# Performance work log

Hardware: AMD Instinct MI355X
Metric: run time of the kernel (lower is better)

The kernel has to match this reference:

```python
import jax, jax.numpy as jnp
import numpy as np

V = 30000   # vocab (from get_word_embedding default)
D = 640     # d_model
L = 6       # num_layers
H = 8       # num_heads
DH = D // H # head dim 80
FF = 4 * D  # ffn hidden 2560
BOS = 1
EOS = 2
LN_EPS = 1e-6


def _ln(x, s, b):
    m = x.mean(-1, keepdims=True)
    v = ((x - m) ** 2).mean(-1, keepdims=True)
    return (x - m) / jnp.sqrt(v + LN_EPS) * s + b


def _get_logits(tokens, seq_len, emb, Wq, bq, Wk, bk, Wv, bv, Wo, bo,
                ln1s, ln1b, W1, b1, W2, b2, ln2s, ln2b, lmW, lmb):
    # tokens: (B,S) int; seq_len: (B,) int
    B, S = tokens.shape
    h = emb[tokens]                                   # (B,S,D), no pos-enc / scaling in source
    look_ahead = jnp.triu(jnp.ones((S, S), jnp.float32), k=1)          # 1 = masked (TF-style)
    pad = (jnp.arange(S)[None, :] >= seq_len[:, None]).astype(jnp.float32)  # (B,S)
    mask = jnp.maximum(look_ahead[None, None, :, :], pad[:, None, None, :])  # (B,1,S,S)

    def layer(h, p):
        wq, bq_, wk, bk_, wv, bv_, wo, bo_, l1s, l1b, w1, b1_, w2, b2_, l2s, l2b = p
        q = (h @ wq + bq_).reshape(B, S, H, DH)
        k = (h @ wk + bk_).reshape(B, S, H, DH)
        v = (h @ wv + bv_).reshape(B, S, H, DH)
        scores = jnp.einsum('bqhd,bkhd->bhqk', q, k) / jnp.sqrt(jnp.float32(DH))
        scores = scores - mask * 1e9
        a = jax.nn.softmax(scores, axis=-1)
        o = jnp.einsum('bhqk,bkhd->bqhd', a, v).reshape(B, S, D) @ wo + bo_
        h = _ln(h + o, l1s, l1b)                      # post-LN residual
        f = jax.nn.relu(h @ w1 + b1_) @ w2 + b2_
        h = _ln(h + f, l2s, l2b)
        return h, None

    h, _ = jax.lax.scan(layer, h, (Wq, bq, Wk, bk, Wv, bv, Wo, bo,
                                   ln1s, ln1b, W1, b1, W2, b2, ln2s, ln2b))
    return h @ lmW + lmb                              # (B,S,V)


def setup_inputs() -> dict:
    key = jax.random.key(0)
    ks = jax.random.split(key, 12)
    std = 0.02

    def n(k, shape):
        return jax.random.normal(k, shape, jnp.float32) * std

    return {
        'initial_words': jax.random.randint(ks[0], (4, 8), 3, V, dtype=jnp.int32),
        'max_length': 32,
        'emb': n(ks[1], (V, D)),
        'Wq': n(ks[2], (L, D, D)), 'bq': jnp.zeros((L, D), jnp.float32),
        'Wk': n(ks[3], (L, D, D)), 'bk': jnp.zeros((L, D), jnp.float32),
        'Wv': n(ks[4], (L, D, D)), 'bv': jnp.zeros((L, D), jnp.float32),
        'Wo': n(ks[5], (L, D, D)), 'bo': jnp.zeros((L, D), jnp.float32),
        'ln1s': jnp.ones((L, D), jnp.float32), 'ln1b': jnp.zeros((L, D), jnp.float32),
        'W1': n(ks[6], (L, D, FF)), 'b1': jnp.zeros((L, FF), jnp.float32),
        'W2': n(ks[7], (L, FF, D)), 'b2': jnp.zeros((L, D), jnp.float32),
        'ln2s': jnp.ones((L, D), jnp.float32), 'ln2b': jnp.zeros((L, D), jnp.float32),
        'lmW': n(ks[8], (D, V)), 'lmb': jnp.zeros((V,), jnp.float32),
    }


def reference(initial_words, max_length, emb, Wq, bq, Wk, bk, Wv, bv, Wo, bo,
              ln1s, ln1b, W1, b1, W2, b2, ln2s, ln2b, lmW, lmb):
    B, init_len = initial_words.shape
    seq_len = jnp.full((B,), max_length, jnp.int32)
    S = max_length + 1  # BOS + max_length slots, as in the torch padding logic
    inp = (jnp.zeros((B, S), jnp.int32)
           .at[:, 0].set(BOS)
           .at[:, 1:1 + init_len].set(initial_words.astype(jnp.int32)))

    def cond(c):
        _inp, cl, tok = c
        return (cl + 1 <= max_length) & jnp.any(tok != EOS)

    def body(c):
        inp, cl, _tok = c
        logits = _get_logits(inp, seq_len, emb, Wq, bq, Wk, bk, Wv, bv, Wo, bo,
                             ln1s, ln1b, W1, b1, W2, b2, ln2s, ln2b, lmW, lmb)
        step_logits = jax.lax.dynamic_index_in_dim(logits, cl, axis=1, keepdims=False)
        tok = jnp.argmax(step_logits, axis=-1).astype(jnp.int32)
        inp = inp.at[:, cl + 1].set(tok)
        return (inp, cl + 1, tok)

    inp, _, _ = jax.lax.while_loop(
        cond, body,
        (inp, jnp.int32(init_len), jnp.full((B,), -100, jnp.int32)))
    return inp[:, 1:]
```

## Files before the change

### kernel.cpp

```cpp
#include <hip/hip_runtime.h>
#include <math.h>

#define B 4
#define SEQ 33
#define MAXLEN 32
#define D 640
#define NH 8
#define DH 80
#define NL 6
#define FF 2560
#define V 30000
#define INITLEN 8
#define NBLK 1024
#define NT 256
#define EOS_TOK 2
#define NPOS_P 9
#define NR_P 36
#define LM_NB 938

#define QKV_N 240
#define AW_B 240
#define AW_E 304
#define F1_B 304
#define F1_E 624
#define F2_B 624
#define F2_E 784

#define NFLAGS 1024
#define NSLOT 32
#define SLOT_U 16

#define VER(t,l) ((size_t)((t) * NL + (l)))

typedef float f4 __attribute__((ext_vector_type(4)));

struct Par {
  const int* iw;
  const float* emb;
  const float *Wq, *bq, *Wk, *bk, *Wv, *bv, *Wo, *bo;
  const float *ln1s, *ln1b, *W1, *b1, *W2, *b2, *ln2s, *ln2b, *lmW, *lmb;
  int* out;
};

__device__ __align__(256) float g_Kc[(size_t)NL * B * NH * SEQ * DH];
__device__ __align__(256) float g_Vc[(size_t)NL * B * NH * SEQ * DH];
__device__ __align__(256) float g_xv[(size_t)SEQ * NL * 2560];
__device__ __align__(256) float g_h1v[(size_t)SEQ * NL * 2560];
__device__ __align__(256) float g_qv[(size_t)SEQ * NL * 2560];
__device__ __align__(256) float g_opartv[(size_t)SEQ * NL * 20480];
__device__ __align__(256) float g_f1v[(size_t)SEQ * NL * 10240];
__device__ __align__(256) float g_f2v[(size_t)SEQ * NL * 5120];
__device__ __align__(256) float g_xlm[(size_t)SEQ * 2560];
__device__ __align__(256) int   g_tokv[SEQ * 64];
__device__ __align__(256) int   g_stopv[SEQ * 64];
__device__ float g_xp[NR_P * D];
__device__ float g_h1p[NR_P * D];
__device__ float g_qkvpP[(size_t)8 * 1920 * NR_P];
__device__ float g_qP[(size_t)NH * NR_P * DH];
__device__ float g_opartP[(size_t)NH * D * NR_P];
__device__ float g_f1pP[(size_t)8 * FF * NR_P];
__device__ float g_f2pP[(size_t)32 * D * NR_P];
__device__ unsigned long long g_keys[(size_t)NBLK * B];
__device__ int g_tokens[B * SEQ];
__device__ unsigned g_flags[(size_t)NFLAGS * NSLOT * SLOT_U];
__device__ unsigned g_arrive = 0;
__device__ unsigned g_gen = 0;

#define KCIDX(l,b,h,pos,j) (((((size_t)(l)*B+(b))*NH+(h))*SEQ+(pos))*DH+(j))

__device__ __forceinline__ float ldc(const float* p) {
  return __hip_atomic_load(p, __ATOMIC_RELAXED, __HIP_MEMORY_SCOPE_AGENT);
}
__device__ __forceinline__ void stc(float* p, float v) {
  __hip_atomic_store(p, v, __ATOMIC_RELAXED, __HIP_MEMORY_SCOPE_AGENT);
}
__device__ __forceinline__ int ldci(const int* p) {
  return __hip_atomic_load(p, __ATOMIC_RELAXED, __HIP_MEMORY_SCOPE_AGENT);
}
__device__ __forceinline__ void stci(int* p, int v) {
  __hip_atomic_store(p, v, __ATOMIC_RELAXED, __HIP_MEMORY_SCOPE_AGENT);
}
__device__ __forceinline__ void stcu64(unsigned long long* p, unsigned long long v) {
  __hip_atomic_store(p, v, __ATOMIC_RELAXED, __HIP_MEMORY_SCOPE_AGENT);
}
__device__ __forceinline__ void st4c(float* p, f4 v) {
  asm volatile("global_store_dwordx4 %0, %1, off sc1" :: "v"(p), "v"(v) : "memory");
}
__device__ __forceinline__ void ld4c_issue(f4& dst, const float* p) {
  asm volatile("global_load_dwordx4 %0, %1, off sc1" : "=v"(dst) : "v"(p) : "memory");
}
__device__ __forceinline__ void wait_vm() {
  asm volatile("s_waitcnt vmcnt(0)" ::: "memory");
  __builtin_amdgcn_sched_barrier(0);
}
__device__ __forceinline__ unsigned long long mk64(float lo, float hi) {
  return ((unsigned long long)__float_as_uint(hi) << 32) | (unsigned long long)__float_as_uint(lo);
}
__device__ __forceinline__ void keep(float x) { asm volatile("" :: "v"(x)); }

__device__ __forceinline__ void gsync_full() {
  __syncthreads();
  if (threadIdx.x == 0) {
    __threadfence();
    unsigned g = __hip_atomic_load(&g_gen, __ATOMIC_SEQ_CST, __HIP_MEMORY_SCOPE_AGENT);
    unsigned old = __hip_atomic_fetch_add(&g_arrive, 1u, __ATOMIC_SEQ_CST, __HIP_MEMORY_SCOPE_AGENT);
    if (old == NBLK - 1u) {
      __hip_atomic_store(&g_arrive, 0u, __ATOMIC_SEQ_CST, __HIP_MEMORY_SCOPE_AGENT);
      __hip_atomic_fetch_add(&g_gen, 1u, __ATOMIC_SEQ_CST, __HIP_MEMORY_SCOPE_AGENT);
    } else {
      while (__hip_atomic_load(&g_gen, __ATOMIC_RELAXED, __HIP_MEMORY_SCOPE_AGENT) == g)
        __builtin_amdgcn_s_sleep(2);
    }
    __threadfence();
  }
  __syncthreads();
}

__device__ __forceinline__ void stage_done(int idx) {
  asm volatile("s_waitcnt vmcnt(0)" ::: "memory");
  __syncthreads();
  if (threadIdx.x == 0) {
    __hip_atomic_fetch_add(
        &g_flags[((size_t)idx * NSLOT + (blockIdx.x & (NSLOT - 1))) * SLOT_U],
        1u, __ATOMIC_RELAXED, __HIP_MEMORY_SCOPE_AGENT);
  }
}

__device__ __forceinline__ void stage_wait(int idx, unsigned cnt) {
  if (threadIdx.x < 64) {
    const unsigned* base = &g_flags[(size_t)idx * NSLOT * SLOT_U];
    int spins = 0;
    for (;;) {
      unsigned v = 0u;
      if (threadIdx.x < NSLOT)
        v = __hip_atomic_load(base + (size_t)threadIdx.x * SLOT_U,
                              __ATOMIC_RELAXED, __HIP_MEMORY_SCOPE_AGENT);
      #pragma unroll
      for (int o = 16; o > 0; o >>= 1) v += __shfl_down(v, o, 64);
      v = __shfl(v, 0, 64);
      if (v >= cnt) break;
      if (spins < 16)       __builtin_amdgcn_s_sleep(1);
      else if (spins < 128) __builtin_amdgcn_s_sleep(8);
      else                  __builtin_amdgcn_s_sleep(32);
      ++spins;
    }
  }
  __syncthreads();
  asm volatile("" ::: "memory");
}

__device__ __forceinline__ float bred_sum(float v, float* s_red) {
  #pragma unroll
  for (int o = 32; o > 0; o >>= 1) v += __shfl_down(v, o, 64);
  __syncthreads();
  if ((threadIdx.x & 63) == 0) s_red[threadIdx.x >> 6] = v;
  __syncthreads();
  return s_red[0] + s_red[1] + s_red[2] + s_red[3];
}

__device__ void ln_inplace(float* row, const float* gam, const float* bet, float* s_red) {
  float ps = 0.f;
  for (int d = threadIdx.x; d < D; d += NT) ps += row[d];
  const float m = bred_sum(ps, s_red) * (1.0f / 640.0f);
  float pv = 0.f;
  for (int d = threadIdx.x; d < D; d += NT) { float t = row[d] - m; pv += t * t; }
  const float var = bred_sum(pv, s_red) * (1.0f / 640.0f);
  const float rstd = 1.0f / sqrtf(var + 1e-6f);
  for (int d = threadIdx.x; d < D; d += NT)
    row[d] = (row[d] - m) * rstd * gam[d] + bet[d];
  __syncthreads();
}

__device__ __forceinline__ void ln_wave(float* s_x, const float* gam, const float* bet) {
  const int tid = threadIdx.x, w = tid >> 6, lane = tid & 63;
  float ps = 0.f;
  for (int i = lane; i < D; i += 64) ps += s_x[w * 640 + i];
  #pragma unroll
  for (int o = 32; o > 0; o >>= 1) ps += __shfl_xor(ps, o, 64);
  const float mean = ps * (1.0f / 640.0f);
  float pv = 0.f;
  for (int i = lane; i < D; i += 64) { float d = s_x[w * 640 + i] - mean; pv += d * d; }
  #pragma unroll
  for (int o = 32; o > 0; o >>= 1) pv += __shfl_xor(pv, o, 64);
  const float rstd = 1.0f / sqrtf(pv * (1.0f / 640.0f) + 1e-6f);
  for (int i = lane; i < D; i += 64)
    s_x[w * 640 + i] = (s_x[w * 640 + i] - mean) * rstd * gam[i] + bet[i];
}

__device__ __forceinline__ void build_x2w(const Par& p, int t, int lsrc, float* s_x) {
  const int tid = threadIdx.x, w = tid >> 6, lane = tid & 63;
  const size_t ver = VER(t, lsrc);
  const float* h1 = g_h1v + ver * 2560 + w * 640;
  const float* fa = g_f2v + ver * 5120 + w * 640;
  const float* fb = g_f2v + ver * 5120 + 2560 + w * 640;
  const float* b2 = p.b2 + (size_t)lsrc * D;
  for (int c4 = lane; c4 < 160; c4 += 64) {
    f4 a = *(const f4*)&h1[c4 * 4];
    f4 b = *(const f4*)&fa[c4 * 4];
    f4 c = *(const f4*)&fb[c4 * 4];
    const float* bb = b2 + c4 * 4;
    f4 s = { a.x + b.x + c.x + bb[0], a.y + b.y + c.y + bb[1],
             a.z + b.z + c.z + bb[2], a.w + b.w + c.w + bb[3] };
    *(f4*)&s_x[w * 640 + c4 * 4] = s;
  }
  ln_wave(s_x, p.ln2s + (size_t)lsrc * D, p.ln2b + (size_t)lsrc * D);
}


__device__ void pf_QKV(const Par& p, int l) {
  const int tid = threadIdx.x;
  const int cg = (blockIdx.x & 7) * 30 + (blockIdx.x >> 3);
  const int m = cg / 80, colm0 = (cg % 80) * 8;
  const int ds = tid >> 3, c = tid & 7;
  const float* Wb = (m == 0 ? p.Wq : m == 1 ? p.Wk : p.Wv)
                    + (size_t)l * D * D + colm0 + c;
  float s = 0.f;
  #pragma unroll
  for (int j = 0; j < 20; ++j) s += Wb[(size_t)(ds + j * 32) * D];
  keep(s);
}

__device__ void pf_AW(const Par& p, int l) {
  const int idx = blockIdx.x - AW_B, h = idx >> 3, c = idx & 7, tid = threadIdx.x;
  if (tid < 240) {
    const int j = tid % 80, sub = tid / 80;
    const int col = c * 80 + j;
    const int d0 = sub * 27, d1 = (sub == 2) ? 80 : d0 + 27;
    const float* Wo = p.Wo + (size_t)l * D * D + col;
    float s = 0.f;
    for (int dd = d0; dd < d1; ++dd) s += Wo[(size_t)(h * 80 + dd) * D];
    keep(s);
  }
}

__device__ void pf_F1(const Par& p, int l) {
  const int tid = threadIdx.x;
  const int raw = blockIdx.x - F1_B;
  const int cg = (raw & 7) * 40 + (raw >> 3);
  const int col0 = cg * 8;
  const int ds = tid >> 3, c = tid & 7;
  const float* Wb = p.W1 + (size_t)l * D * FF + col0 + c;
  float s = 0.f;
  #pragma unroll
  for (int j = 0; j < 20; ++j) s += Wb[(size_t)(ds + j * 32) * FF];
  keep(s);
}

__device__ void pf_F2(const Par& p, int l) {
  const int idx = blockIdx.x - F2_B, tid = threadIdx.x;
  const int hf = idx / 80, craw = idx % 80;
  const int cg = (craw & 7) * 10 + (craw >> 3);
  const int col0 = cg * 8;
  const int ds = tid >> 3, c = tid & 7;
  const float* Wb = p.W2 + (size_t)l * FF * D + (size_t)hf * 1280 * D + col0 + c;
  float s = 0.f;
  #pragma unroll
  for (int kb = 0; kb < 40; ++kb) s += Wb[(size_t)(ds + kb * 32) * D];
  keep(s);
}

__device__ void pf_LM(const Par& p) {
  const int bid = blockIdx.x, tid = threadIdx.x;
  const int xcd = bid & 7, jj = bid >> 3;
  const int chunk = (xcd < 2 ? xcd * 118 : 236 + (xcd - 2) * 117) + jj;
  const int sg = tid >> 5, cj = tid & 31;
  const int col = chunk * 32 + cj;
  if (col < V) {
    const float* W = p.lmW + (size_t)sg * 80 * V + col;
    float s = 0.f;
    for (int kb = 0; kb < 80; ++kb) s += W[(size_t)kb * V];
    keep(s);
  }
}


__device__ void st_QKV(const Par& p, int l, int t, float* s_x, float* s_t, float* s_r) {
  const int tid = threadIdx.x;
  const int cg = (blockIdx.x & 7) * 30 + (blockIdx.x >> 3);
  const int m = cg / 80, colm0 = (cg % 80) * 8;
  const int w = tid >> 6, lane = tid & 63;
  if (l == 0) {
    const int tok = g_tokv[t * 64 + w];
    for (int c4 = lane; c4 < 160; c4 += 64)
      *(f4*)&s_x[w * 640 + c4 * 4] = *(const f4*)&p.emb[(size_t)tok * D + c4 * 4];
  } else {
    build_x2w(p, t, l - 1, s_x);
  }
  __syncthreads();
  if (cg == 0) {
    const size_t xo = VER(t, l) * 2560;
    for (int i = tid; i < 640; i += NT)
      st4c(&g_xv[xo + (size_t)i * 4], *(f4*)&s_x[i * 4]);
  }
  const int ds = tid >> 3, c = tid & 7;
  const float* Wb = (m == 0 ? p.Wq : m == 1 ? p.Wk : p.Wv)
                    + (size_t)l * D * D + colm0 + c;
  float a0 = 0, a1 = 0, a2 = 0, a3 = 0;
  {
    float wv[20];
    #pragma unroll
    for (int j = 0; j < 20; ++j) wv[j] = Wb[(size_t)(ds + j * 32) * D];
    #pragma unroll
    for (int j = 0; j < 20; ++j) {
      const int dd = ds + j * 32;
      a0 = fmaf(s_x[dd],        wv[j], a0);
      a1 = fmaf(s_x[640 + dd],  wv[j], a1);
      a2 = fmaf(s_x[1280 + dd], wv[j], a2);
      a3 = fmaf(s_x[1920 + dd], wv[j], a3);
    }
  }
  { f4 av = { a0, a1, a2, a3 }; *(f4*)&s_t[c * 132 + ds * 4] = av; }
  __syncthreads();
  if (tid < 32) {
    const int c2 = tid >> 2, b = tid & 3;
    float v = 0.f;
    #pragma unroll
    for (int d2 = 0; d2 < 32; ++d2) v += s_t[c2 * 132 + d2 * 4 + b];
    v += (m == 0 ? p.bq : m == 1 ? p.bk : p.bv)[(size_t)l * D + colm0 + c2];
    s_r[c2 * 4 + b] = v;
  }
  __syncthreads();
  if (m == 0) {
    if (tid < 8) {
      f4 v = { s_r[tid * 4], s_r[tid * 4 + 1], s_r[tid * 4 + 2], s_r[tid * 4 + 3] };
      st4c(&g_qv[VER(t, l) * 2560 + (size_t)(colm0 + tid) * 4], v);
    }
  } else {
    const int h = colm0 / 80, j0 = colm0 % 80;
    if (tid < 8) {
      const int b = tid >> 1, cq4 = (tid & 1) * 4;
      f4 v = { s_r[(cq4+0)*4+b], s_r[(cq4+1)*4+b], s_r[(cq4+2)*4+b], s_r[(cq4+3)*4+b] };
      float* cache = (m == 1) ? g_Kc : g_Vc;
      st4c(&cache[KCIDX(l, b, h, t, j0 + cq4)], v);
    }
  }
}

__device__ void st_AW(const Par& p, int l, int t,
                      float* s_q, float* s_sc, float* s_o, float* s_wo) {
  const int idx = blockIdx.x - AW_B, h = idx >> 3, c = idx & 7, tid = threadIdx.x;
  const size_t qo = VER(t, l) * 2560;
  if (tid < 80) {
    f4 q = *(const f4*)&g_qv[qo + (size_t)(h * 80 + tid) * 4];
    s_q[tid] = q.x; s_q[80 + tid] = q.y; s_q[160 + tid] = q.z; s_q[240 + tid] = q.w;
  }
  __syncthreads();
  const int nk = t + 1;
  for (int task = tid; task < 4 * nk; task += NT) {
    const int b = task / nk, kp = task % nk;
    const float* qq = s_q + b * 80;
    const f4* kk = (const f4*)&g_Kc[KCIDX(l, b, h, kp, 0)];
    float sd = 0.f;
    #pragma unroll
    for (int j4 = 0; j4 < 20; ++j4) {
      f4 k4 = kk[j4];
      sd += qq[j4*4+0]*k4.x + qq[j4*4+1]*k4.y + qq[j4*4+2]*k4.z + qq[j4*4+3]*k4.w;
    }
    s_sc[b * 33 + kp] = sd / 8.94427190999915878564f;
  }
  __syncthreads();
  if (tid < 4) {
    const int b = tid;
    float m = -1e30f;
    for (int k = 0; k < nk; ++k) m = fmaxf(m, s_sc[b * 33 + k]);
    float sum = 0.f;
    for (int k = 0; k < nk; ++k) { float e = expf(s_sc[b * 33 + k] - m); s_sc[b * 33 + k] = e; sum += e; }
    s_sc[132 + b] = 1.0f / sum;
  }
  __syncthreads();
  if (tid < 80) {
    const int b = tid / 20, j4 = tid % 20;
    f4 acc = { 0.f, 0.f, 0.f, 0.f };
    for (int kp = 0; kp < nk; ++kp) {
      f4 v = *(const f4*)&g_Vc[KCIDX(l, b, h, kp, j4 * 4)];
      const float wgt = s_sc[b * 33 + kp];
      acc.x += wgt * v.x; acc.y += wgt * v.y; acc.z += wgt * v.z; acc.w += wgt * v.w;
    }
    const float r = s_sc[132 + b];
    f4 o = { acc.x * r, acc.y * r, acc.z * r, acc.w * r };
    *(f4*)&s_o[b * 80 + j4 * 4] = o;
  }
  __syncthreads();
  if (tid < 240) {
    const int j = tid % 80, sub = tid / 80;
    const int col = c * 80 + j;
    const int d0 = sub * 27, d1 = (sub == 2) ? 80 : d0 + 27;
    const float* Wo = p.Wo + (size_t)l * D * D + col;
    float a0 = 0, a1 = 0, a2 = 0, a3 = 0;
    #pragma unroll 9
    for (int dd = d0; dd < d1; ++dd) {
      const float w = Wo[(size_t)(h * 80 + dd) * D];
      a0 += s_o[0*80+dd] * w; a1 += s_o[80+dd] * w;
      a2 += s_o[160+dd] * w; a3 += s_o[240+dd] * w;
    }
    float* tp = s_wo + (j * 3 + sub) * 4;
    tp[0] = a0; tp[1] = a1; tp[2] = a2; tp[3] = a3;
  }
  __syncthreads();
  if (tid < 80) {
    const int b = tid / 20, cq = tid % 20;
    f4 v;
    #pragma unroll
    for (int i = 0; i < 4; ++i) {
      const int j = cq * 4 + i;
      v[i] = s_wo[(j*3+0)*4+b] + s_wo[(j*3+1)*4+b] + s_wo[(j*3+2)*4+b];
    }
    st4c(&g_opartv[VER(t, l) * 20480 + (size_t)(h * 4 + b) * 640 + c * 80 + cq * 4], v);
  }
}

__device__ void st_F1(const Par& p, int l, int t, float* s_x, float* s_t, float* s_r) {
  const int tid = threadIdx.x;
  const int raw = blockIdx.x - F1_B;
  const int cg = (raw & 7) * 40 + (raw >> 3);
  const int col0 = cg * 8;
  const size_t ver = VER(t, l);
  const int w = tid >> 6, lane = tid & 63;
  {
    const float* xv = g_xv + ver * 2560 + w * 640;
    const float* bo = p.bo + (size_t)l * D;
    for (int c4 = lane; c4 < 160; c4 += 64) {
      f4 a = *(const f4*)&xv[c4 * 4];
      const float* bb = bo + c4 * 4;
      a.x += bb[0]; a.y += bb[1]; a.z += bb[2]; a.w += bb[3];
      #pragma unroll
      for (int h = 0; h < 8; ++h) {
        f4 ov = *(const f4*)&g_opartv[ver * 20480 + (size_t)(h * 4 + w) * 640 + c4 * 4];
        a.x += ov.x; a.y += ov.y; a.z += ov.z; a.w += ov.w;
      }
      *(f4*)&s_x[w * 640 + c4 * 4] = a;
    }
    ln_wave(s_x, p.ln1s + (size_t)l * D, p.ln1b + (size_t)l * D);
  }
  __syncthreads();
  if (raw == 0) {
    for (int i = tid; i < 640; i += NT)
      st4c(&g_h1v[ver * 2560 + (size_t)i * 4], *(f4*)&s_x[i * 4]);
  }
  const int ds = tid >> 3, c = tid & 7;
  const float* Wb = p.W1 + (size_t)l * D * FF + col0 + c;
  float a0 = 0, a1 = 0, a2 = 0, a3 = 0;
  {
    float wv[20];
    #pragma unroll
    for (int j = 0; j < 20; ++j) wv[j] = Wb[(size_t)(ds + j * 32) * FF];
    #pragma unroll
    for (int j = 0; j < 20; ++j) {
      const int dd = ds + j * 32;
      a0 = fmaf(s_x[dd],        wv[j], a0);
      a1 = fmaf(s_x[640 + dd],  wv[j], a1);
      a2 = fmaf(s_x[1280 + dd], wv[j], a2);
      a3 = fmaf(s_x[1920 + dd], wv[j], a3);
    }
  }
  { f4 av = { a0, a1, a2, a3 }; *(f4*)&s_t[c * 132 + ds * 4] = av; }
  __syncthreads();
  if (tid < 32) {
    const int c2 = tid >> 2, b = tid & 3;
    float v = 0.f;
    #pragma unroll
    for (int d2 = 0; d2 < 32; ++d2) v += s_t[c2 * 132 + d2 * 4 + b];
    v += p.b1[(size_t)l * FF + col0 + c2];
    s_r[c2 * 4 + b] = fmaxf(v, 0.f);
  }
  __syncthreads();
  if (tid < 8) {
    const int b = tid >> 1, cq4 = (tid & 1) * 4;
    f4 v = { s_r[(cq4+0)*4+b], s_r[(cq4+1)*4+b], s_r[(cq4+2)*4+b], s_r[(cq4+3)*4+b] };
    st4c(&g_f1v[ver * 10240 + (size_t)b * 2560 + col0 + cq4], v);
  }
}

__device__ void st_F2(const Par& p, int l, int t, float* s_f, float* s_t, float* s_r) {
  const int idx = blockIdx.x - F2_B, tid = threadIdx.x;
  const int hf = idx / 80, craw = idx % 80;
  const int cg = (craw & 7) * 10 + (craw >> 3);
  const int col0 = cg * 8;
  const size_t ver = VER(t, l);
  #pragma unroll
  for (int i = 0; i < 5; ++i) {
    const int ii = tid + i * NT;
    const int b = ii / 320, fo = ii % 320;
    *(f4*)&s_f[b * 1280 + fo * 4] =
        *(const f4*)&g_f1v[ver * 10240 + (size_t)b * 2560 + hf * 1280 + fo * 4];
  }
  __syncthreads();
  const int ds = tid >> 3, c = tid & 7;
  const float* Wb = p.W2 + (size_t)l * FF * D + (size_t)hf * 1280 * D + col0 + c;
  float a0 = 0, a1 = 0, a2 = 0, a3 = 0;
  #pragma unroll
  for (int kb = 0; kb < 40; kb += 20) {
    float wv[20];
    #pragma unroll
    for (int j = 0; j < 20; ++j) wv[j] = Wb[(size_t)(ds + (kb + j) * 32) * D];
    #pragma unroll
    for (int j = 0; j < 20; ++j) {
      const int dl = ds + (kb + j) * 32;
      a0 = fmaf(s_f[dl],        wv[j], a0);
      a1 = fmaf(s_f[1280 + dl], wv[j], a1);
      a2 = fmaf(s_f[2560 + dl], wv[j], a2);
      a3 = fmaf(s_f[3840 + dl], wv[j], a3);
    }
  }
  { f4 av = { a0, a1, a2, a3 }; *(f4*)&s_t[c * 132 + ds * 4] = av; }
  __syncthreads();
  if (tid < 32) {
    const int c2 = tid >> 2, b = tid & 3;
    float v = 0.f;
    #pragma unroll
    for (int d2 = 0; d2 < 32; ++d2) v += s_t[c2 * 132 + d2 * 4 + b];
    s_r[c2 * 4 + b] = v;
  }
  __syncthreads();
  if (tid < 8) {
    const int b = tid >> 1, cq4 = (tid & 1) * 4;
    f4 v = { s_r[(cq4+0)*4+b], s_r[(cq4+1)*4+b], s_r[(cq4+2)*4+b], s_r[(cq4+3)*4+b] };
    st4c(&g_f2v[ver * 5120 + (size_t)(hf * 4 + b) * 640 + col0 + cq4], v);
  }
}

__device__ void st_LM(const Par& p, int t, int src, float* s_xf, float* s_part,
                      unsigned long long* s_key) {
  const int bid = blockIdx.x, tid = threadIdx.x;
  const int xcd = bid & 7, jj = bid >> 3;
  const int chunk = (xcd < 2 ? xcd * 118 : 236 + (xcd - 2) * 117) + jj;
  if (src == 0) {
    #pragma unroll
    for (int i = 0; i < 3; ++i) {
      const int idx = tid + i * NT;
      if (idx < 640) *(f4*)&s_xf[idx * 4] = *(const f4*)&g_xlm[(size_t)t * 2560 + (size_t)idx * 4];
    }
  } else {
    build_x2w(p, t, NL - 1, s_xf);
  }
  __syncthreads();
  const int sg = tid >> 5, cj = tid & 31;
  const int col = chunk * 32 + cj;
  float a0 = 0, a1 = 0, a2 = 0, a3 = 0;
  if (col < V) {
    const float* W = p.lmW + (size_t)sg * 80 * V + col;
    #pragma unroll
    for (int kb = 0; kb < 80; kb += 20) {
      float w[20];
      #pragma unroll
      for (int j = 0; j < 20; ++j) w[j] = W[(size_t)(kb + j) * V];
      #pragma unroll
      for (int j = 0; j < 20; ++j) {
        const int d = sg * 80 + kb + j;
        a0 = fmaf(s_xf[d],        w[j], a0);
        a1 = fmaf(s_xf[640 + d],  w[j], a1);
        a2 = fmaf(s_xf[1280 + d], w[j], a2);
        a3 = fmaf(s_xf[1920 + d], w[j], a3);
      }
    }
  }
  float* tp = s_part + (sg * 32 + cj) * 4;
  tp[0] = a0; tp[1] = a1; tp[2] = a2; tp[3] = a3;
  __syncthreads();
  if (tid < 128) {
    const int cj2 = tid >> 2, b = tid & 3, col2 = chunk * 32 + cj2;
    unsigned long long key = 0ull;
    if (col2 < V) {
      float a = p.lmb[col2];
      #pragma unroll
      for (int sg2 = 0; sg2 < 8; ++sg2) a += s_part[(sg2 * 32 + cj2) * 4 + b];
      unsigned u = __float_as_uint(a);
      u = (u & 0x80000000u) ? ~u : (u | 0x80000000u);
      key = ((unsigned long long)u << 32) | (unsigned)(V - col2);
    }
    s_key[cj2 * 4 + b] = key;
  }
  __syncthreads();
  if (tid < 4) {
    unsigned long long k0 = 0ull;
    for (int cj2 = 0; cj2 < 32; ++cj2) {
      const unsigned long long k = s_key[cj2 * 4 + tid];
      if (k > k0) k0 = k;
    }
    stcu64(&g_keys[(size_t)bid * B + tid], k0);
  }
}

__device__ void st_CTL(int t, unsigned long long* s_k64, int* s_ctl) {
  const int tid = threadIdx.x;
  const int i0 = tid, i1 = tid + NT, i2 = tid + 2 * NT, i3 = tid + 3 * NT;
  f4 z = { 0.f, 0.f, 0.f, 0.f };
  f4 ka0, kb0, ka1, kb1, ka2, kb2, ka3 = z, kb3 = z;
  ld4c_issue(ka0, (const float*)&g_keys[(size_t)i0 * 4]);
  ld4c_issue(kb0, (const float*)&g_keys[(size_t)i0 * 4 + 2]);
  ld4c_issue(ka1, (const float*)&g_keys[(size_t)i1 * 4]);
  ld4c_issue(kb1, (const float*)&g_keys[(size_t)i1 * 4 + 2]);
  ld4c_issue(ka2, (const float*)&g_keys[(size_t)i2 * 4]);
  ld4c_issue(kb2, (const float*)&g_keys[(size_t)i2 * 4 + 2]);
  if (i3 < LM_NB) {
    ld4c_issue(ka3, (const float*)&g_keys[(size_t)i3 * 4]);
    ld4c_issue(kb3, (const float*)&g_keys[(size_t)i3 * 4 + 2]);
  }
  wait_vm();
  unsigned long long m0 = mk64(ka0.x, ka0.y), m1 = mk64(ka0.z, ka0.w);
  unsigned long long m2 = mk64(kb0.x, kb0.y), m3 = mk64(kb0.z, kb0.w);
  { unsigned long long s;
    s = mk64(ka1.x,ka1.y); if (s>m0) m0=s;  s = mk64(ka1.z,ka1.w); if (s>m1) m1=s;
    s = mk64(kb1.x,kb1.y); if (s>m2) m2=s;  s = mk64(kb1.z,kb1.w); if (s>m3) m3=s;
    s = mk64(ka2.x,ka2.y); if (s>m0) m0=s;  s = mk64(ka2.z,ka2.w); if (s>m1) m1=s;
    s = mk64(kb2.x,kb2.y); if (s>m2) m2=s;  s = mk64(kb2.z,kb2.w); if (s>m3) m3=s;
    s = mk64(ka3.x,ka3.y); if (s>m0) m0=s;  s = mk64(ka3.z,ka3.w); if (s>m1) m1=s;
    s = mk64(kb3.x,kb3.y); if (s>m2) m2=s;  s = mk64(kb3.z,kb3.w); if (s>m3) m3=s;
  }
  #pragma unroll
  for (int o = 32; o > 0; o >>= 1) {
    unsigned long long s;
    s = __shfl_down(m0, o, 64); if (s > m0) m0 = s;
    s = __shfl_down(m1, o, 64); if (s > m1) m1 = s;
    s = __shfl_down(m2, o, 64); if (s > m2) m2 = s;
    s = __shfl_down(m3, o, 64); if (s > m3) m3 = s;
  }
  if ((tid & 63) == 0) {
    const int w = tid >> 6;
    s_k64[w * 4 + 0] = m0; s_k64[w * 4 + 1] = m1;
    s_k64[w * 4 + 2] = m2; s_k64[w * 4 + 3] = m3;
  }
  __syncthreads();
  if (tid == 0) {
    #pragma unroll
    for (int b = 0; b < B; ++b) {
      unsigned long long k0 = s_k64[b];
      #pragma unroll
      for (int w = 1; w < 4; ++w) if (s_k64[w * 4 + b] > k0) k0 = s_k64[w * 4 + b];
      const int tok = V - (int)(unsigned)(k0 & 0xFFFFFFFFull);
      stci(&g_tokens[b * SEQ + t + 1], tok);
      stci(&g_tokv[(t + 1) * 64 + b], tok);
      s_ctl[b] = tok;
    }
    int stop = (t == MAXLEN - 1) ? 1 : 0;
    if (s_ctl[0] == EOS_TOK && s_ctl[1] == EOS_TOK &&
        s_ctl[2] == EOS_TOK && s_ctl[3] == EOS_TOK) stop = 1;
    stci(&g_stopv[t * 64], stop);
  }
}


__device__ void st_Qp(const Par& p, int l, float* s_a) {
  const int idx = blockIdx.x, tid = threadIdx.x;
  const int h = idx / 24, rem = idx % 24, s = rem / 3, rg = rem % 3;
  const int r0 = rg * 12, d0 = s * 80;
  for (int i = tid; i < 960; i += NT) {
    const int ri = i / 80, dd = i % 80;
    s_a[i] = ldc(&g_xp[(r0 + ri) * D + d0 + dd]);
  }
  __syncthreads();
  if (tid < 240) {
    const int m = tid / 80, j = tid % 80, col = h * 80 + j;
    const float* W = (m == 0 ? p.Wq : m == 1 ? p.Wk : p.Wv) + (size_t)l * D * D + col;
    float acc[12];
    #pragma unroll
    for (int ri = 0; ri < 12; ++ri) acc[ri] = 0.f;
    for (int dd = 0; dd < 80; ++dd) {
      const float w = W[(size_t)(d0 + dd) * D];
      #pragma unroll
      for (int ri = 0; ri < 12; ++ri) acc[ri] += s_a[ri * 80 + dd] * w;
    }
    float* o = g_qkvpP + ((size_t)s * 1920 + m * 640 + col) * NR_P + r0;
    #pragma unroll
    for (int ri = 0; ri < 12; ++ri) stc(o + ri, acc[ri]);
  }
}

__device__ void st_AWp1(const Par& p, int l) {
  const int idx = blockIdx.x - 192, h = idx >> 2, c = idx & 3, tid = threadIdx.x;
  for (int pp = c; pp < NPOS_P; pp += 4) {
    for (int task = tid; task < 960; task += NT) {
      const int m = task / 320, rem = task % 320, j = rem >> 2, b = rem & 3;
      const int r = pp * 4 + b;
      const int col = m * 640 + h * 80 + j;
      const float* q = g_qkvpP + (size_t)col * NR_P + r;
      float a = 0.f;
      #pragma unroll
      for (int s = 0; s < 8; ++s) a += ldc(q + (size_t)s * 1920 * NR_P);
      a += (m == 0 ? p.bq : m == 1 ? p.bk : p.bv)[(size_t)l * D + h * 80 + j];
      if (m == 0)      stc(&g_qP[((size_t)h * NR_P + r) * DH + j], a);
      else if (m == 1) stc(&g_Kc[KCIDX(l, b, h, pp, j)], a);
      else             stc(&g_Vc[KCIDX(l, b, h, pp, j)], a);
    }
  }
}

__device__ void st_AWp2(const Par& p, int l, float* s_a, float* s_b, float* s_c) {
  const int idx = blockIdx.x - 224, h = idx >> 2, rg = idx & 3, tid = threadIdx.x;
  const int r0 = rg * 9;
  for (int i = tid; i < 720; i += NT) {
    const int ri = i / 80, j = i % 80;
    s_a[i] = ldc(&g_qP[((size_t)h * NR_P + r0 + ri) * DH + j]);
  }
  __syncthreads();
  for (int task = tid; task < 81; task += NT) {
    const int ri = task / 9, kp = task % 9;
    const int r = r0 + ri, pos = r >> 2, b = r & 3;
    if (kp <= pos) {
      const float* kk = g_Kc + KCIDX(l, b, h, kp, 0);
      const float* qq = s_a + ri * 80;
      float sd = 0.f;
      for (int j = 0; j < 80; ++j) sd += qq[j] * ldc(kk + j);
      s_c[ri * 9 + kp] = sd / 8.94427190999915878564f;
    }
  }
  __syncthreads();
  if (tid < 9) {
    const int ri = tid, r = r0 + ri, pos = r >> 2;
    float m = -1e30f;
    for (int k = 0; k <= pos; ++k) m = fmaxf(m, s_c[ri * 9 + k]);
    float sum = 0.f;
    for (int k = 0; k <= pos; ++k) { float e = expf(s_c[ri * 9 + k] - m); s_c[ri * 9 + k] = e; sum += e; }
    s_c[81 + ri] = 1.0f / sum;
  }
  __syncthreads();
  for (int task = tid; task < 720; task += NT) {
    const int ri = task / 80, j = task % 80;
    const int r = r0 + ri, pos = r >> 2, b = r & 3;
    float acc = 0.f;
    for (int kp = 0; kp <= pos; ++kp)
      acc += s_c[ri * 9 + kp] * ldc(&g_Vc[KCIDX(l, b, h, kp, j)]);
    s_b[ri * 80 + j] = acc * s_c[81 + ri];
  }
  __syncthreads();
  if (tid < 160) {
    for (int pass = 0; pass < 4; ++pass) {
      const int col = pass * 160 + tid;
      const float* Wo = p.Wo + (size_t)l * D * D + col;
      float acc[9];
      #pragma unroll
      for (int ri = 0; ri < 9; ++ri) acc[ri] = 0.f;
      for (int dd = 0; dd < 80; ++dd) {
        const float w = Wo[(size_t)(h * 80 + dd) * D];
        #pragma unroll
        for (int ri = 0; ri < 9; ++ri) acc[ri] += s_b[ri * 80 + dd] * w;
      }
      #pragma unroll
      for (int ri = 0; ri < 9; ++ri)
        stc(&g_opartP[((size_t)h * D + col) * NR_P + r0 + ri], acc[ri]);
    }
  }
}

__device__ void st_RFp(const Par& p, int l, float* s_row, float* s_red) {
  const int r = blockIdx.x, tid = threadIdx.x;
  for (int col = tid; col < D; col += NT) {
    float a = ldc(&g_xp[r * D + col]) + p.bo[(size_t)l * D + col];
    #pragma unroll
    for (int h = 0; h < 8; ++h) a += ldc(&g_opartP[((size_t)h * D + col) * NR_P + r]);
    s_row[col] = a;
  }
  __syncthreads();
  ln_inplace(s_row, p.ln1s + (size_t)l * D, p.ln1b + (size_t)l * D, s_red);
  for (int col = tid; col < D; col += NT) stc(&g_h1p[r * D + col], s_row[col]);
}

__device__ void st_F1p(const Par& p, int l, float* s_a) {
  const int idx = blockIdx.x, tid = threadIdx.x;
  const int s = idx / 30, rem = idx % 30, cg = rem / 3, rg = rem % 3;
  const int r0 = rg * 12, d0 = s * 80;
  for (int i = tid; i < 960; i += NT) {
    const int ri = i / 80, dd = i % 80;
    s_a[i] = ldc(&g_h1p[(r0 + ri) * D + d0 + dd]);
  }
  __syncthreads();
  const int col = cg * 256 + tid;
  const float* W = p.W1 + (size_t)l * D * FF + col;
  float acc[12];
  #pragma unroll
  for (int ri = 0; ri < 12; ++ri) acc[ri] = 0.f;
  for (int dd = 0; dd < 80; ++dd) {
    const float w = W[(size_t)(d0 + dd) * FF];
    #pragma unroll
    for (int ri = 0; ri < 12; ++ri) acc[ri] += s_a[ri * 80 + dd] * w;
  }
  float* o = g_f1pP + ((size_t)s * FF + col) * NR_P + r0;
  #pragma unroll
  for (int ri = 0; ri < 12; ++ri) stc(o + ri, acc[ri]);
}

__device__ void st_F2p(const Par& p, int l, float* s_c) {
  const int idx = blockIdx.x - 240, c = idx / 3, rg = idx % 3, tid = threadIdx.x;
  const int r0 = rg * 12;
  for (int task = tid; task < 960; task += NT) {
    const int ri = task / 80, fj = task % 80;
    const int fcol = c * 80 + fj;
    const float* pp = g_f1pP + (size_t)fcol * NR_P + r0 + ri;
    float a = 0.f;
    #pragma unroll
    for (int s = 0; s < 8; ++s) a += ldc(pp + (size_t)s * FF * NR_P);
    a += p.b1[(size_t)l * FF + fcol];
    s_c[ri * 80 + fj] = fmaxf(a, 0.f);
  }
  __syncthreads();
  for (int pass = 0; pass < 3; ++pass) {
    const int col = pass * 256 + tid;
    if (col < D) {
      const float* W = p.W2 + (size_t)l * FF * D + col;
      float acc[12];
      #pragma unroll
      for (int ri = 0; ri < 12; ++ri) acc[ri] = 0.f;
      for (int fj = 0; fj < 80; ++fj) {
        const float w = W[(size_t)(c * 80 + fj) * D];
        #pragma unroll
        for (int ri = 0; ri < 12; ++ri) acc[ri] += s_c[ri * 80 + fj] * w;
      }
      float* o = g_f2pP + ((size_t)c * D + col) * NR_P + r0;
      #pragma unroll
      for (int ri = 0; ri < 12; ++ri) stc(o + ri, acc[ri]);
    }
  }
}

__device__ void st_RQp(const Par& p, int l, float* s_row, float* s_red) {
  const int r = blockIdx.x, tid = threadIdx.x;
  for (int col = tid; col < D; col += NT) {
    float a = ldc(&g_h1p[r * D + col]) + p.b2[(size_t)l * D + col];
    #pragma unroll 8
    for (int c = 0; c < 32; ++c) a += ldc(&g_f2pP[((size_t)c * D + col) * NR_P + r]);
    s_row[col] = a;
  }
  __syncthreads();
  ln_inplace(s_row, p.ln2s + (size_t)l * D, p.ln2b + (size_t)l * D, s_red);
  for (int col = tid; col < D; col += NT) stc(&g_xp[r * D + col], s_row[col]);
}

__device__ void st_RLp(const Par& p, float* s_row, float* s_red) {
  const int b = blockIdx.x, r = 32 + b, tid = threadIdx.x;
  for (int col = tid; col < D; col += NT) {
    float a = ldc(&g_h1p[r * D + col]) + p.b2[(size_t)(NL - 1) * D + col];
    #pragma unroll 8
    for (int c = 0; c < 32; ++c) a += ldc(&g_f2pP[((size_t)c * D + col) * NR_P + r]);
    s_row[col] = a;
  }
  __syncthreads();
  ln_inplace(s_row, p.ln2s + (size_t)(NL - 1) * D, p.ln2b + (size_t)(NL - 1) * D, s_red);
  for (int col = tid; col < D; col += NT)
    stc(&g_xlm[(size_t)INITLEN * 2560 + (size_t)b * 640 + col], s_row[col]);
}

__global__ __launch_bounds__(NT, 4) void tfgen(Par p) {
  __shared__ float s_pool[6400];
  __shared__ float s_red[8];
  __shared__ unsigned long long s_key[128];
  __shared__ int s_ctl[8];

  const int bid = blockIdx.x, tid = threadIdx.x;
  int ep = 0;

  {
    unsigned* f = g_flags + (size_t)bid * NSLOT * SLOT_U;
    for (int i = tid; i < NSLOT * SLOT_U; i += NT) f[i] = 0u;
  }
  if (bid < NR_P) {
    const int pos = bid >> 2, b = bid & 3;
    const int tk = (pos == 0) ? 1 : p.iw[b * INITLEN + pos - 1];
    for (int d = tid; d < D; d += NT) stc(&g_xp[bid * D + d], p.emb[(size_t)tk * D + d]);
  }
  if (bid == NBLK - 1) {
    for (int i = tid; i < B * SEQ; i += NT) {
      const int b = i / SEQ, pos = i % SEQ;
      int tk = 0;
      if (pos == 0) tk = 1;
      else if (pos <= INITLEN) tk = p.iw[b * INITLEN + pos - 1];
      stci(&g_tokens[i], tk);
    }
  }
  gsync_full();

  float* ps_x  = s_pool;
  float* ps_a  = s_pool + 2560;
  float* ps_b  = s_pool + 3584;
  float* ps_c  = s_pool + 4352;
  int eRQ = -1, eF2last = -1;
  for (int l = 0; l < NL; ++l) {
    const int eQ = ep++;
    if (bid < 192) { if (l > 0) stage_wait(eRQ, 36); st_Qp(p, l, ps_a); stage_done(eQ); }
    const int eA1 = ep++;
    if (bid >= 192 && bid < 224) { stage_wait(eQ, 192); st_AWp1(p, l); stage_done(eA1); }
    const int eA2 = ep++;
    if (bid >= 224 && bid < 256) { stage_wait(eA1, 32); st_AWp2(p, l, ps_a, ps_b, ps_c); stage_done(eA2); }
    const int eRF = ep++;
    if (bid < NR_P) { stage_wait(eA2, 32); st_RFp(p, l, ps_x, s_red); stage_done(eRF); }
    const int eF1 = ep++;
    if (bid < 240) { stage_wait(eRF, 36); st_F1p(p, l, ps_a); stage_done(eF1); }
    const int eF2 = ep++;
    if (bid >= 240 && bid < 336) { stage_wait(eF1, 240); st_F2p(p, l, ps_c); stage_done(eF2); }
    eF2last = eF2;
    if (l < NL - 1) {
      eRQ = ep++;
      if (bid < NR_P) { stage_wait(eF2, 96); st_RQp(p, l, ps_x, s_red); stage_done(eRQ); }
    }
  }

  for (int t = INITLEN;; ++t) {
    int eCTL;
    if (t == INITLEN) {
      const int eRLp = ep++;
      if (bid < 4) { stage_wait(eF2last, 96); st_RLp(p, s_pool, s_red); stage_done(eRLp); }
      const int eLM = ep++;
      if (bid < LM_NB) { pf_LM(p); stage_wait(eRLp, 4); st_LM(p, t, 0, s_pool, s_pool + 2560, s_key); stage_done(eLM); }
      eCTL = ep++;
      if (bid == NBLK - 1) { stage_wait(eLM, LM_NB); st_CTL(t, s_key, s_ctl); stage_done(eCTL); }
    } else {
      int eF2s = -1;
      for (int l = 0; l < NL; ++l) {
        const int eQKV = ep++;
        if (bid < QKV_N) {
          if (l > 0) { pf_QKV(p, l); stage_wait(eF2s, 160); }
          st_QKV(p, l, t, s_pool, s_pool + 2560, s_pool + 3648);
          stage_done(eQKV);
        }
        const int eAW = ep++;
        if (bid >= AW_B && bid < AW_E) {
          pf_AW(p, l);
          stage_wait(eQKV, QKV_N);
          st_AW(p, l, t, s_pool, s_pool + 320, s_pool + 480, s_pool + 800);
          stage_done(eAW);
        }
        const int eF1 = ep++;
        if (bid >= F1_B && bid < F1_E) {
          pf_F1(p, l);
          stage_wait(eAW, 64);
          st_F1(p, l, t, s_pool, s_pool + 2560, s_pool + 3648);
          stage_done(eF1);
        }
        eF2s = ep++;
        if (bid >= F2_B && bid < F2_E) {
          pf_F2(p, l);
          stage_wait(eF1, 320);
          st_F2(p, l, t, s_pool, s_pool + 5120, s_pool + 6208);
          stage_done(eF2s);
        }
      }
      const int eLM = ep++;
      if (bid < LM_NB) {
        pf_LM(p);
        stage_wait(eF2s, 160);
        st_LM(p, t, 1, s_pool, s_pool + 2560, s_key);
        stage_done(eLM);
      }
      eCTL = ep++;
      if (bid == NBLK - 1) { stage_wait(eLM, LM_NB); st_CTL(t, s_key, s_ctl); stage_done(eCTL); }
    }
    if (bid < QKV_N) pf_QKV(p, 0);
    stage_wait(eCTL, 1);
    if (g_stopv[t * 64]) break;
  }

  if (bid == 0) {
    for (int i = tid; i < B * MAXLEN; i += NT) {
      const int b = i >> 5, j = i & 31;
      p.out[i] = ldci(&g_tokens[b * SEQ + j + 1]);
    }
  }
}

extern "C" void kernel_launch(void* const* d_in, const int* in_sizes, int n_in,
                              void* d_out, int out_size, void* d_ws, size_t ws_size,
                              hipStream_t stream)
{
  (void)in_sizes; (void)n_in; (void)out_size; (void)d_ws; (void)ws_size;
  Par p;
  p.iw   = (const int*)  d_in[0];
  p.emb  = (const float*)d_in[2];
  p.Wq   = (const float*)d_in[3];  p.bq   = (const float*)d_in[4];
  p.Wk   = (const float*)d_in[5];  p.bk   = (const float*)d_in[6];
  p.Wv   = (const float*)d_in[7];  p.bv   = (const float*)d_in[8];
  p.Wo   = (const float*)d_in[9];  p.bo   = (const float*)d_in[10];
  p.ln1s = (const float*)d_in[11]; p.ln1b = (const float*)d_in[12];
  p.W1   = (const float*)d_in[13]; p.b1   = (const float*)d_in[14];
  p.W2   = (const float*)d_in[15]; p.b2   = (const float*)d_in[16];
  p.ln2s = (const float*)d_in[17]; p.ln2b = (const float*)d_in[18];
  p.lmW  = (const float*)d_in[19]; p.lmb  = (const float*)d_in[20];
  p.out  = (int*)d_out;

  void* args[] = { (void*)&p };
  hipError_t err = hipLaunchCooperativeKernel((const void*)tfgen, dim3(NBLK), dim3(NT),
                                              args, 0, stream);
  if (err != hipSuccess) {
    hipLaunchKernelGGL(tfgen, dim3(NBLK), dim3(NT), 0, stream, p);
  }
}
```

Measured before the change: 17.02 ms.

## Replace CTL stage barrier with direct stop-flag poll, drop LM prefetch, tune spin

Blocks no longer wait on a separate CTL stage counter. Each block now has one thread poll the per-step stop word, which st_CTL writes as a nonzero valid-plus-stop value after a vmcnt wait, and the result is broadcast through shared memory. This removes one flag-sum stage per decode step. The LM-head weight prefetch pass is also removed, and the spin-wait backoff now starts with a few sleep-free polls. The stop words are zeroed at init. Risks include heavier polling traffic on one address and colder lmW reads in the LM stage.

```diff
diff --git a/kernel.cpp b/kernel.cpp
--- a/kernel.cpp
+++ b/kernel.cpp
@@ -139,8 +139,9 @@
       for (int o = 16; o > 0; o >>= 1) v += __shfl_down(v, o, 64);
       v = __shfl(v, 0, 64);
       if (v >= cnt) break;
-      if (spins < 16)       __builtin_amdgcn_s_sleep(1);
-      else if (spins < 128) __builtin_amdgcn_s_sleep(8);
+      if (spins < 8)        {  }
+      else if (spins < 64)  __builtin_amdgcn_s_sleep(1);
+      else if (spins < 192) __builtin_amdgcn_s_sleep(8);
       else                  __builtin_amdgcn_s_sleep(32);
       ++spins;
     }
@@ -259,20 +260,6 @@
   keep(s);
 }
 
-__device__ void pf_LM(const Par& p) {
-  const int bid = blockIdx.x, tid = threadIdx.x;
-  const int xcd = bid & 7, jj = bid >> 3;
-  const int chunk = (xcd < 2 ? xcd * 118 : 236 + (xcd - 2) * 117) + jj;
-  const int sg = tid >> 5, cj = tid & 31;
-  const int col = chunk * 32 + cj;
-  if (col < V) {
-    const float* W = p.lmW + (size_t)sg * 80 * V + col;
-    float s = 0.f;
-    for (int kb = 0; kb < 80; ++kb) s += W[(size_t)kb * V];
-    keep(s);
-  }
-}
-
 
 __device__ void st_QKV(const Par& p, int l, int t, float* s_x, float* s_t, float* s_r) {
   const int tid = threadIdx.x;
@@ -635,7 +622,8 @@
     int stop = (t == MAXLEN - 1) ? 1 : 0;
     if (s_ctl[0] == EOS_TOK && s_ctl[1] == EOS_TOK &&
         s_ctl[2] == EOS_TOK && s_ctl[3] == EOS_TOK) stop = 1;
-    stci(&g_stopv[t * 64], stop);
+    asm volatile("s_waitcnt vmcnt(0)" ::: "memory");
+    stci(&g_stopv[t * 64], 1 | (stop << 1));
   }
 }
 
@@ -865,6 +853,7 @@
       else if (pos <= INITLEN) tk = p.iw[b * INITLEN + pos - 1];
       stci(&g_tokens[i], tk);
     }
+    for (int i = tid; i < SEQ; i += NT) stci(&g_stopv[i * 64], 0);
   }
   gsync_full();
 
@@ -894,14 +883,12 @@
   }
 
   for (int t = INITLEN;; ++t) {
-    int eCTL;
     if (t == INITLEN) {
       const int eRLp = ep++;
       if (bid < 4) { stage_wait(eF2last, 96); st_RLp(p, s_pool, s_red); stage_done(eRLp); }
       const int eLM = ep++;
-      if (bid < LM_NB) { pf_LM(p); stage_wait(eRLp, 4); st_LM(p, t, 0, s_pool, s_pool + 2560, s_key); stage_done(eLM); }
-      eCTL = ep++;
-      if (bid == NBLK - 1) { stage_wait(eLM, LM_NB); st_CTL(t, s_key, s_ctl); stage_done(eCTL); }
+      if (bid < LM_NB) { stage_wait(eRLp, 4); st_LM(p, t, 0, s_pool, s_pool + 2560, s_key); stage_done(eLM); }
+      if (bid == NBLK - 1) { stage_wait(eLM, LM_NB); st_CTL(t, s_key, s_ctl); }
     } else {
       int eF2s = -1;
       for (int l = 0; l < NL; ++l) {
@@ -934,18 +921,24 @@
         }
       }
       const int eLM = ep++;
-      if (bid < LM_NB) {
-        pf_LM(p);
-        stage_wait(eF2s, 160);
-        st_LM(p, t, 1, s_pool, s_pool + 2560, s_key);
-        stage_done(eLM);
+      if (bid < LM_NB) { stage_wait(eF2s, 160); st_LM(p, t, 1, s_pool, s_pool + 2560, s_key); stage_done(eLM); }
+      if (bid == NBLK - 1) { stage_wait(eLM, LM_NB); st_CTL(t, s_key, s_ctl); }
+    }
+    if (bid < QKV_N) pf_QKV(p, 0);
+    if (tid == 0) {
+      int v, spins = 0;
+      while ((v = ldci(&g_stopv[t * 64])) == 0) {
+        if (spins < 8)        {  }
+        else if (spins < 64)  __builtin_amdgcn_s_sleep(1);
+        else if (spins < 192) __builtin_amdgcn_s_sleep(8);
+        else                  __builtin_amdgcn_s_sleep(32);
+        ++spins;
       }
-      eCTL = ep++;
-      if (bid == NBLK - 1) { stage_wait(eLM, LM_NB); st_CTL(t, s_key, s_ctl); stage_done(eCTL); }
-    }
-    if (bid < QKV_N) pf_QKV(p, 0);
-    stage_wait(eCTL, 1);
-    if (g_stopv[t * 64]) break;
+      s_ctl[4] = v;
+    }
+    __syncthreads();
+    asm volatile("" ::: "memory");
+    if (s_ctl[4] >> 1) break;
   }
 
   if (bid == 0) {
```

Result: faster. 15.92 ms, median of 2 (-6.5%).
